# Performance work log

Measured on AMD Instinct MI355X. Metric: run time of the kernel, lower is better.

The kernel has to match this reference:

```python
import jax, jax.numpy as jnp
import numpy as np

# Winograd F(4x4, 3x3) transform matrices (m=4, r=3, a=6)
B_T = jnp.array([[4.,0.,-5.,0.,1.,0.],
                 [0.,-4.,-4.,1.,1.,0.],
                 [0.,4.,-4.,-1.,1.,0.],
                 [0.,-2.,-1.,2.,1.,0.],
                 [0.,2.,-1.,-2.,1.,0.],
                 [0.,4.,0.,-5.,0.,1.]], dtype=jnp.float32)
G = jnp.array([[1/4.,0.,0.],
               [-1/6.,-1/6.,-1/6.],
               [-1/6.,1/6.,-1/6.],
               [1/24.,1/12.,1/6.],
               [1/24.,-1/12.,1/6.],
               [0.,0.,1.]], dtype=jnp.float32)
A_T = jnp.array([[1.,1.,1.,1.,1.,0.],
                 [0.,1.,-1.,2.,-2.,0.],
                 [0.,1.,1.,4.,4.,0.],
                 [0.,1.,-1.,8.,-8.,1.]], dtype=jnp.float32)

M_OUT, R_K, A_IN = 4, 3, 6  # output tile m, kernel r, input tile a = m+r-1


def setup_inputs() -> dict:
    key = jax.random.key(0)
    k1, k2 = jax.random.split(key)
    x = jax.random.normal(k1, (16, 64, 130, 130), dtype=jnp.float32)
    w = jax.random.normal(k2, (64, 64, 3, 3), dtype=jnp.float32) * 0.05
    return {"input": x, "weight": w}


def reference(input, weight):
    N, C, H, W = input.shape
    K = weight.shape[0]
    m, r, a = M_OUT, R_K, A_IN
    T = (H - r + 1) // m  # tiles per spatial dim (perfect tiling)

    # Filter transform: U[k,c] = G @ w[k,c] @ G^T  -> [K,C,a,a]
    U = jnp.einsum('ai,kcij,bj->kcab', G, weight, G)

    # Extract overlapping a x a input tiles with stride m: [N,C,T,a,T,a]
    idx = (jnp.arange(T) * m)[:, None] + jnp.arange(a)[None, :]  # [T,a]
    tiles = input[:, :, idx, :][:, :, :, :, idx]

    # Input transform: V = B^T @ tile @ B  -> [N,T,T,C,a,a]
    V = jnp.einsum('ai,nctisj,bj->ntscab', B_T, tiles, B_T)
    Vp = V.reshape(N * T * T, C, a, a)  # [P,C,a,a]

    # Elementwise (tile-domain) multiply + channel reduce: M[p,k] = sum_c U[k,c]*V[p,c]
    Mt = jnp.einsum('kcab,pcab->pkab', U, Vp)  # [P,K,a,a]

    # Output transform: Y_tile = A^T @ M @ A -> [P,K,m,m]
    Yt = jnp.einsum('ai,pkij,bj->pkab', A_T, Mt, A_T)

    out = T * m  # = H - r + 1
    Y = Yt.reshape(N, T, T, K, m, m).transpose(0, 3, 1, 4, 2, 5).reshape(N, K, out, out)
    return Y
```

## Files before the change

### kernel.cpp

```cpp
#include <hip/hip_runtime.h>


__constant__ float c_AT[24] = {
  1.f, 0.f, 0.f, 0.f,
  1.f, 1.f, 1.f, 1.f,
  1.f,-1.f, 1.f,-1.f,
  1.f, 2.f, 4.f, 8.f,
  1.f,-2.f, 4.f,-8.f,
  0.f, 0.f, 0.f, 1.f
};

__device__ __forceinline__ void gl2lds16(const float* g, float* l) {
  __builtin_amdgcn_global_load_lds((const __attribute__((address_space(1))) void*)g,
                                   (__attribute__((address_space(3))) void*)l, 16, 0, 0);
}

__global__ __launch_bounds__(256) void k_filter(const float* __restrict__ w,
                                                float* __restrict__ U) {
  int g = blockIdx.x * 256 + threadIdx.x;
  int k = g & 63;
  int c = g >> 6;
  const float* wp = w + (size_t)(k * 64 + c) * 9;
  float w00 = wp[0], w01 = wp[1], w02 = wp[2];
  float w10 = wp[3], w11 = wp[4], w12 = wp[5];
  float w20 = wp[6], w21 = wp[7], w22 = wp[8];
  const float G[6][3] = {
    {0.25f, 0.f, 0.f},
    {-1.f/6.f, -1.f/6.f, -1.f/6.f},
    {-1.f/6.f,  1.f/6.f, -1.f/6.f},
    {1.f/24.f,  1.f/12.f, 1.f/6.f},
    {1.f/24.f, -1.f/12.f, 1.f/6.f},
    {0.f, 0.f, 1.f}
  };
  float t[6][3];
#pragma unroll
  for (int a = 0; a < 6; ++a) {
    t[a][0] = G[a][0]*w00 + G[a][1]*w10 + G[a][2]*w20;
    t[a][1] = G[a][0]*w01 + G[a][1]*w11 + G[a][2]*w21;
    t[a][2] = G[a][0]*w02 + G[a][1]*w12 + G[a][2]*w22;
  }
#pragma unroll
  for (int a = 0; a < 6; ++a) {
#pragma unroll
    for (int b = 0; b < 6; ++b) {
      float u = G[b][0]*t[a][0] + G[b][1]*t[a][1] + G[b][2]*t[a][2];
      U[(size_t)(a*6+b)*4096 + c*64 + k] = u;
    }
  }
}

__global__ __launch_bounds__(256) void k_input(const float* __restrict__ x,
                                               float* __restrict__ V,
                                               int n0, int Pchunk) {
  __shared__ float Ls[34*134];
  const int tid  = threadIdx.x;
  const int bi   = blockIdx.x;
  const int band = bi & 3;
  const int c    = (bi >> 2) & 63;
  const int nl   = bi >> 8;
  const float* xp = x + (size_t)((n0 + nl) * 64 + c) * (130*130) + band * 32 * 130;
  for (int idx = tid; idx < 34*65; idx += 256) {
    int r  = idx / 65;
    int c2 = idx - r * 65;
    *(float2*)&Ls[r*134 + c2*2] = *(const float2*)(xp + r*130 + c2*2);
  }
  __syncthreads();
  const int tyl = tid >> 5;
  const int tx  = tid & 31;
  const int ty  = band * 8 + tyl;
  const int p   = (nl * 32 + ty) * 32 + tx;
  const float* bl = &Ls[(tyl*4)*134 + tx*4];
  float t1[6][6];
#pragma unroll
  for (int j = 0; j < 6; ++j) {
    float d0 = bl[0*134+j], d1 = bl[1*134+j], d2 = bl[2*134+j];
    float d3 = bl[3*134+j], d4 = bl[4*134+j], d5 = bl[5*134+j];
    t1[0][j] =  4.f*d0 - 5.f*d2 + d4;
    t1[1][j] = -4.f*d1 - 4.f*d2 + d3 + d4;
    t1[2][j] =  4.f*d1 - 4.f*d2 - d3 + d4;
    t1[3][j] = -2.f*d1 -     d2 + 2.f*d3 + d4;
    t1[4][j] =  2.f*d1 -     d2 - 2.f*d3 + d4;
    t1[5][j] =  4.f*d1 - 5.f*d3 + d5;
  }
  float* vb = V + (size_t)c * Pchunk + p;
  const size_t abs_ = (size_t)64 * Pchunk;
#pragma unroll
  for (int a = 0; a < 6; ++a) {
    float s0=t1[a][0], s1=t1[a][1], s2=t1[a][2], s3=t1[a][3], s4=t1[a][4], s5=t1[a][5];
    float v0 =  4.f*s0 - 5.f*s2 + s4;
    float v1 = -4.f*s1 - 4.f*s2 + s3 + s4;
    float v2 =  4.f*s1 - 4.f*s2 - s3 + s4;
    float v3 = -2.f*s1 -     s2 + 2.f*s3 + s4;
    float v4 =  2.f*s1 -     s2 - 2.f*s3 + s4;
    float v5 =  4.f*s1 - 5.f*s3 + s5;
    vb[(size_t)(a*6+0)*abs_] = v0;
    vb[(size_t)(a*6+1)*abs_] = v1;
    vb[(size_t)(a*6+2)*abs_] = v2;
    vb[(size_t)(a*6+3)*abs_] = v3;
    vb[(size_t)(a*6+4)*abs_] = v4;
    vb[(size_t)(a*6+5)*abs_] = v5;
  }
}

__global__ __launch_bounds__(256) void k_gemm2(const float* __restrict__ V,
                                               const float* __restrict__ U,
                                               float* __restrict__ M,
                                               int Pchunk, int nPB) {
  __shared__ float Vs[64*256];
  __shared__ float Us[64*64];
  const int tid  = threadIdx.x;
  const int lane = tid & 63;
  const int wv   = tid >> 6;
  const unsigned bx = blockIdx.x;
  const int ab = bx / (unsigned)nPB;
  const int pb = bx - ab * nPB;
  const int p0 = pb * 256;

  const float* Vab = V + (size_t)ab * 64 * Pchunk + p0;
  const float* Uab = U + (size_t)ab * 4096;

#pragma unroll
  for (int i = 0; i < 16; ++i) {
    int r = wv + i * 4;
    gl2lds16(Vab + (size_t)r * Pchunk + lane * 4, &Vs[r * 256]);
  }
#pragma unroll
  for (int i = 0; i < 4; ++i) {
    int li = wv + i * 4;
    gl2lds16(Uab + li * 256 + lane * 4, &Us[li * 256]);
  }
  __syncthreads();

  const int pt = tid & 31;
  const int kt = tid >> 5;
  float acc[8][8];
#pragma unroll
  for (int ki = 0; ki < 8; ++ki)
#pragma unroll
    for (int pi = 0; pi < 8; ++pi) acc[ki][pi] = 0.f;

#pragma unroll 4
  for (int c = 0; c < 64; ++c) {
    const float4 va = *(const float4*)&Vs[c*256 + pt*4];
    const float4 vb = *(const float4*)&Vs[c*256 + 128 + pt*4];
    const float4 ua = *(const float4*)&Us[c*64 + kt*8];
    const float4 ub = *(const float4*)&Us[c*64 + kt*8 + 4];
    const float vv[8] = {va.x, va.y, va.z, va.w, vb.x, vb.y, vb.z, vb.w};
    const float uu[8] = {ua.x, ua.y, ua.z, ua.w, ub.x, ub.y, ub.z, ub.w};
#pragma unroll
    for (int ki = 0; ki < 8; ++ki)
#pragma unroll
      for (int pi = 0; pi < 8; ++pi)
        acc[ki][pi] += uu[ki] * vv[pi];
  }

#pragma unroll
  for (int ki = 0; ki < 8; ++ki) {
    float* mb = M + ((size_t)ab * 64 + kt*8 + ki) * Pchunk + p0;
    *(float4*)(mb + pt*4)       = make_float4(acc[ki][0], acc[ki][1], acc[ki][2], acc[ki][3]);
    *(float4*)(mb + 128 + pt*4) = make_float4(acc[ki][4], acc[ki][5], acc[ki][6], acc[ki][7]);
  }
}

__global__ __launch_bounds__(256) void k_out(const float* __restrict__ M,
                                             float* __restrict__ out,
                                             int n0, int Pchunk, int bpk) {
  const unsigned bx = blockIdx.x;
  const int k    = bx / (unsigned)bpk;
  const int pblk = bx - k * bpk;
  const int p    = pblk * 256 + threadIdx.x;
  const int nl = p >> 10;
  const int ty = (p >> 5) & 31;
  const int tx = p & 31;

  const float* mp = M + (size_t)k * Pchunk + p;
  const size_t abstride = (size_t)64 * Pchunk;
  float m[36];
#pragma unroll
  for (int ab = 0; ab < 36; ++ab) m[ab] = mp[(size_t)ab * abstride];

  float Y[4][4];
#pragma unroll
  for (int u = 0; u < 4; ++u)
#pragma unroll
    for (int v = 0; v < 4; ++v) Y[u][v] = 0.f;

#pragma unroll
  for (int i = 0; i < 6; ++i) {
    float R[4] = {0.f, 0.f, 0.f, 0.f};
#pragma unroll
    for (int j = 0; j < 6; ++j) {
      float mm = m[i*6 + j];
#pragma unroll
      for (int v = 0; v < 4; ++v) R[v] += c_AT[j*4 + v] * mm;
    }
#pragma unroll
    for (int u = 0; u < 4; ++u) {
      float au = c_AT[i*4 + u];
#pragma unroll
      for (int v = 0; v < 4; ++v) Y[u][v] += au * R[v];
    }
  }

  float* ob = out + ((size_t)((n0 + nl) * 64 + k) * 128 + ty*4) * 128 + tx*4;
#pragma unroll
  for (int u = 0; u < 4; ++u)
    *(float4*)(ob + (size_t)u * 128) = make_float4(Y[u][0], Y[u][1], Y[u][2], Y[u][3]);
}

extern "C" void kernel_launch(void* const* d_in, const int* in_sizes, int n_in,
                              void* d_out, int out_size, void* d_ws, size_t ws_size,
                              hipStream_t stream) {
  const float* x = (const float*)d_in[0];
  const float* w = (const float*)d_in[1];
  float* out = (float*)d_out;
  float* U = (float*)d_ws;
  const size_t U_bytes = 36ull * 64 * 64 * 4;
  const size_t per_n = 2ull * 36 * 1024 * 64 * 4;
  size_t avail = ws_size > U_bytes ? ws_size - U_bytes : 0;
  int chunk = (int)(avail / per_n);
  if (chunk < 1) return;
  if (chunk > 16) chunk = 16;

  k_filter<<<16, 256, 0, stream>>>(w, U);
  for (int n0 = 0; n0 < 16; n0 += chunk) {
    int cn = (16 - n0) < chunk ? (16 - n0) : chunk;
    int Pchunk = cn * 1024;
    float* V = (float*)((char*)d_ws + U_bytes);
    float* M = V + (size_t)36 * 64 * Pchunk;
    int nPB = cn * 4;
    k_input<<<cn*256,  256, 0, stream>>>(x, V, n0, Pchunk);
    k_gemm2<<<36*nPB,  256, 0, stream>>>(V, U, M, Pchunk, nPB);
    k_out  <<<64*nPB,  256, 0, stream>>>(M, out, n0, Pchunk, nPB);
  }
}
```

Before: 268.3 us.

## Double-buffer GEMM channel tiles in LDS and cap batch chunk at eight

The tile-domain GEMM no longer loads all 64 channels of V and U into LDS before computing. It now splits them into four 16-channel stages with two LDS buffers, prefetching the next stage while the current one is computed, which hides global-to-LDS load latency and halves LDS use per block so more blocks can be resident. Separately, the host caps the batch chunk at 8 images instead of up to 16, giving two passes with a smaller V/M working set that may stay in cache better. The trade-offs are more barriers per block and an extra round of kernel launches.

After: 261.9 us. 2.4% less time.

```diff
diff --git a/kernel.cpp b/kernel.cpp
--- a/kernel.cpp
+++ b/kernel.cpp
@@ -106,8 +106,8 @@
                                                const float* __restrict__ U,
                                                float* __restrict__ M,
                                                int Pchunk, int nPB) {
-  __shared__ float Vs[64*256];
-  __shared__ float Us[64*64];
+  __shared__ float Vs[2][16*256];
+  __shared__ float Us[2][16*64];
   const int tid  = threadIdx.x;
   const int lane = tid & 63;
   const int wv   = tid >> 6;
@@ -119,17 +119,16 @@
   const float* Vab = V + (size_t)ab * 64 * Pchunk + p0;
   const float* Uab = U + (size_t)ab * 4096;
 
-#pragma unroll
-  for (int i = 0; i < 16; ++i) {
-    int r = wv + i * 4;
-    gl2lds16(Vab + (size_t)r * Pchunk + lane * 4, &Vs[r * 256]);
-  }
-#pragma unroll
-  for (int i = 0; i < 4; ++i) {
-    int li = wv + i * 4;
-    gl2lds16(Uab + li * 256 + lane * 4, &Us[li * 256]);
-  }
-  __syncthreads();
+  auto stage = [&](int cc, int b) {
+#pragma unroll
+    for (int i = 0; i < 4; ++i) {
+      int rl = wv * 4 + i;
+      gl2lds16(Vab + (size_t)(cc * 16 + rl) * Pchunk + lane * 4, &Vs[b][rl * 256]);
+    }
+    gl2lds16(Uab + cc * 1024 + wv * 256 + lane * 4, &Us[b][wv * 256]);
+  };
+
+  stage(0, 0);
 
   const int pt = tid & 31;
   const int kt = tid >> 5;
@@ -139,19 +138,27 @@
 #pragma unroll
     for (int pi = 0; pi < 8; ++pi) acc[ki][pi] = 0.f;
 
+  __syncthreads();
+
+#pragma unroll
+  for (int cc = 0; cc < 4; ++cc) {
+    const int b = cc & 1;
+    if (cc < 3) stage(cc + 1, b ^ 1);
 #pragma unroll 4
-  for (int c = 0; c < 64; ++c) {
-    const float4 va = *(const float4*)&Vs[c*256 + pt*4];
-    const float4 vb = *(const float4*)&Vs[c*256 + 128 + pt*4];
-    const float4 ua = *(const float4*)&Us[c*64 + kt*8];
-    const float4 ub = *(const float4*)&Us[c*64 + kt*8 + 4];
-    const float vv[8] = {va.x, va.y, va.z, va.w, vb.x, vb.y, vb.z, vb.w};
-    const float uu[8] = {ua.x, ua.y, ua.z, ua.w, ub.x, ub.y, ub.z, ub.w};
-#pragma unroll
-    for (int ki = 0; ki < 8; ++ki)
-#pragma unroll
-      for (int pi = 0; pi < 8; ++pi)
-        acc[ki][pi] += uu[ki] * vv[pi];
+    for (int c = 0; c < 16; ++c) {
+      const float4 va = *(const float4*)&Vs[b][c*256 + pt*4];
+      const float4 vb = *(const float4*)&Vs[b][c*256 + 128 + pt*4];
+      const float4 ua = *(const float4*)&Us[b][c*64 + kt*8];
+      const float4 ub = *(const float4*)&Us[b][c*64 + kt*8 + 4];
+      const float vv[8] = {va.x, va.y, va.z, va.w, vb.x, vb.y, vb.z, vb.w};
+      const float uu[8] = {ua.x, ua.y, ua.z, ua.w, ub.x, ub.y, ub.z, ub.w};
+#pragma unroll
+      for (int ki = 0; ki < 8; ++ki)
+#pragma unroll
+        for (int pi = 0; pi < 8; ++pi)
+          acc[ki][pi] += uu[ki] * vv[pi];
+    }
+    __syncthreads();
   }
 
 #pragma unroll
@@ -218,9 +225,9 @@
   const size_t U_bytes = 36ull * 64 * 64 * 4;
   const size_t per_n = 2ull * 36 * 1024 * 64 * 4;
   size_t avail = ws_size > U_bytes ? ws_size - U_bytes : 0;
-  int chunk = (int)(avail / per_n);
-  if (chunk < 1) return;
-  if (chunk > 16) chunk = 16;
+  int chunk = 8;
+  while (chunk > 1 && per_n * (size_t)chunk > avail) chunk >>= 1;
+  if (per_n > avail) return;
 
   k_filter<<<16, 256, 0, stream>>>(w, U);
   for (int n0 = 0; n0 < 16; n0 += chunk) {
```
